# Kernel optimization log

Hardware: AMD Instinct MI355X
Metric: run time of the kernel (lower is better)

## Reference

```python
import jax, jax.numpy as jnp
import numpy as np

N_NODES = 100000
N_EDGES = 1600000
F_IN, F_HID, F_OUT = 48, 16, 16
K = 2  # kernel_size, dim=1, degree=1 open B-spline -> basis (1-u, u)


def glorot(key, shape):
    fan_in, fan_out = shape[-2], shape[-1]
    s = jnp.sqrt(6.0 / (fan_in + fan_out))
    return jax.random.uniform(key, shape, jnp.float32, -s, s)


def setup_inputs() -> dict:
    key = jax.random.key(0)
    ks = jax.random.split(key, 10)
    x = jax.random.normal(ks[0], (N_NODES, F_IN), jnp.float32)
    edge_attr = jax.random.uniform(ks[1], (N_EDGES, 1), jnp.float32)
    edge_index = jax.random.randint(ks[2], (2, N_EDGES), 0, N_NODES, jnp.int64)
    W1 = glorot(ks[3], (K, F_IN, F_HID))
    root1 = glorot(ks[4], (F_IN, F_HID))
    b1 = jnp.zeros((F_HID,), jnp.float32)
    W2 = glorot(ks[5], (K, F_HID, F_OUT))
    root2 = glorot(ks[6], (F_HID, F_OUT))
    b2 = jnp.zeros((F_OUT,), jnp.float32)
    return {"x": x, "edge_attr": edge_attr, "edge_index": edge_index,
            "W1": W1, "root1": root1, "b1": b1, "W2": W2, "root2": root2, "b2": b2}


def spline_conv(x, edge_index, u, W, root, bias, num_nodes):
    # x: [N,Fin], u: [E] pseudo coords in [0,1], W: [2,Fin,Fout]
    src, dst = edge_index[0], edge_index[1]
    xj = x[src]                                        # [E,Fin] gather
    m = jnp.einsum('ef,kfo->eko', xj, W)               # [E,2,Fout]
    basis = jnp.stack([1.0 - u, u], axis=1)            # linear open B-spline, K=2
    msg = jnp.einsum('ek,eko->eo', basis, m)           # [E,Fout]
    agg = jax.ops.segment_sum(msg, dst, num_segments=num_nodes)
    cnt = jax.ops.segment_sum(jnp.ones_like(msg[:, 0]), dst, num_segments=num_nodes)
    agg = agg / jnp.maximum(cnt, 1.0)[:, None]         # aggr='mean'
    return agg + x @ root + bias                       # root_weight + bias


def reference(x, edge_attr, edge_index, W1, root1, b1, W2, root2, b2):
    u = edge_attr[:, 0]
    h = jax.nn.elu(spline_conv(x, edge_index, u, W1, root1, b1, N_NODES))
    out = spline_conv(h, edge_index, u, W2, root2, b2, N_NODES)
    return jax.nn.log_softmax(out, axis=1)
```

## Files before the change

kernel.cpp:

```cpp
#include <hip/hip_runtime.h>
#include <math.h>

#define N_NODES 100000
#define N_EDGES 1600000
#define NBUK 782
#define BNODES 128
#define CAP 2560
#define CAPB (CAP * 8)
#define NCHUNK 512
#define CPE 3125
#define NTBLK 1563
#define WS 52
#define RPW (BNODES + 1)

#define SM_LCUR  0
#define SM_GBASE 3128
#define SM_SC    6256
#define SM_UPDL  10352
#define SM_SPDL  35352
#define SM_TOTAL 60352

#define NTL(p) __builtin_nontemporal_load(p)

__device__ __forceinline__ unsigned bf16_rne(float x) {
    unsigned u = __float_as_uint(x);
    return (u + 0x7FFFu + ((u >> 16) & 1u)) >> 16;
}

__device__ __forceinline__ void accq(float acc[4], uint4 w, float uu) {
    acc[0] += fmaf(uu, __uint_as_float(w.x & 0xFFFF0000u), __uint_as_float(w.x << 16));
    acc[1] += fmaf(uu, __uint_as_float(w.y & 0xFFFF0000u), __uint_as_float(w.y << 16));
    acc[2] += fmaf(uu, __uint_as_float(w.z & 0xFFFF0000u), __uint_as_float(w.z << 16));
    acc[3] += fmaf(uu, __uint_as_float(w.w & 0xFFFF0000u), __uint_as_float(w.w << 16));
}

__global__ __launch_bounds__(1024)
void fused_transform_scatter(const float* __restrict__ X,
                             const float* __restrict__ W,
                             const float* __restrict__ root,
                             const float* __restrict__ bias,
                             unsigned* __restrict__ YPH, float* __restrict__ R,
                             const int* __restrict__ src,
                             const int* __restrict__ dst,
                             const float* __restrict__ u,
                             int* __restrict__ cursor,
                             unsigned long long* __restrict__ pkd) {
    extern __shared__ char smem[];
    int t = threadIdx.x;
    if (blockIdx.x < NCHUNK) {
        int c = blockIdx.x;
        int* lcur = (int*)(smem + SM_LCUR);
        int* gbase = (int*)(smem + SM_GBASE);
        int* sc = (int*)(smem + SM_SC);
        unsigned long long* updl = (unsigned long long*)(smem + SM_UPDL);
        unsigned long long* spdl = (unsigned long long*)(smem + SM_SPDL);

        for (int i = t; i < NBUK; i += 1024) lcur[i] = 0;
        __syncthreads();
        for (int j = t; j < CPE; j += 1024) {
            int e = c * CPE + j;
            int d = NTL(dst + e);
            float uu = NTL(u + e);
            uu = uu < 0.0f ? 0.0f : (uu > 1.0f ? 1.0f : uu);
            int u15 = (int)fmaf(uu, 32767.0f, 0.5f);
            unsigned pk32 = (unsigned)NTL(src + e) | ((unsigned)u15 << 17);
            updl[j] = (unsigned long long)pk32 |
                      ((unsigned long long)(unsigned)d << 32);
            atomicAdd(&lcur[d >> 7], 1);
        }
        __syncthreads();

        int v = (t < NBUK) ? lcur[t] : 0;
        sc[t] = v;
        __syncthreads();
        for (int off = 1; off < 1024; off <<= 1) {
            int x = (t >= off) ? sc[t - off] : 0;
            __syncthreads();
            sc[t] += x;
            __syncthreads();
        }
        if (t < NBUK) {
            int ex = sc[t] - v;
            lcur[t] = ex;
            int base = t * CAP + atomicAdd(&cursor[t], v);
            gbase[t] = base - ex;
        }
        __syncthreads();

        for (int j = t; j < CPE; j += 1024) {
            unsigned long long w = updl[j];
            int b = (int)(w >> 39) & 0x3FF;
            int p = atomicAdd(&lcur[b], 1);
            spdl[p] = w;
        }
        __syncthreads();

        for (int j = t; j < CPE; j += 1024) {
            unsigned long long w = spdl[j];
            int b = (int)(w >> 39) & 0x3FF;
            int g = gbase[b] + j;
            if (g < (b + 1) * CAP)
                pkd[g] = w;
        }
    } else {
        float* sW0 = (float*)smem;
        float* sWd = (float*)(smem + 3328);
        float* sR  = (float*)(smem + 6656);
        float* sB  = (float*)(smem + 9984);
        int bid = blockIdx.x - NCHUNK;
        for (int i = t; i < 48 * 16; i += 1024) {
            int f = i >> 4, o = i & 15;
            float w0 = W[i];
            float w1 = W[48 * 16 + i];
            sW0[o * WS + f] = w0;
            sWd[o * WS + f] = w1 - w0;
            sR[o * WS + f]  = root[i];
        }
        if (t < 16) sB[t] = bias[t];
        __syncthreads();

        int idx = bid * 1024 + t;
        int n = idx >> 4;
        int o = idx & 15;
        if (n >= N_NODES) return;

        const float4* xr  = (const float4*)(X + (long)n * 48);
        const float4* w0p = (const float4*)(sW0 + o * WS);
        const float4* wdp = (const float4*)(sWd + o * WS);
        const float4* wrp = (const float4*)(sR  + o * WS);
        float a0 = 0.0f, a1 = 0.0f, ar = 0.0f;
#pragma unroll
        for (int fc = 0; fc < 12; ++fc) {
            float4 xv = xr[fc];
            float4 w0 = w0p[fc];
            float4 wd = wdp[fc];
            float4 wr = wrp[fc];
            a0 = fmaf(xv.x, w0.x, a0); a0 = fmaf(xv.y, w0.y, a0);
            a0 = fmaf(xv.z, w0.z, a0); a0 = fmaf(xv.w, w0.w, a0);
            a1 = fmaf(xv.x, wd.x, a1); a1 = fmaf(xv.y, wd.y, a1);
            a1 = fmaf(xv.z, wd.z, a1); a1 = fmaf(xv.w, wd.w, a1);
            ar = fmaf(xv.x, wr.x, ar); ar = fmaf(xv.y, wr.y, ar);
            ar = fmaf(xv.z, wr.z, ar); ar = fmaf(xv.w, wr.w, ar);
        }
        YPH[idx] = bf16_rne(a0) | (bf16_rne(a1) << 16);
        R[idx]   = ar + sB[o];
    }
}

__global__ __launch_bounds__(512)
void aggregate1(const int* __restrict__ cursor,
                unsigned long long* __restrict__ pkd,
                int* __restrict__ rptab,
                const uint4* __restrict__ YPH1,
                const float* __restrict__ R1,
                const float* __restrict__ W2,
                const float* __restrict__ root2,
                const float* __restrict__ b2,
                unsigned* __restrict__ YPH2,
                float* __restrict__ R2) {
    __shared__ unsigned long long updl[CAP];
    __shared__ unsigned spk[CAP];
    __shared__ int rp[RPW];
    __shared__ int cur[BNODES];
    __shared__ float sW0[256], sWd[256], sR[256], sB[16];
    int t = threadIdx.x, b = blockIdx.x;

    if (t < 256) {
        float w0 = W2[t], w1 = W2[256 + t];
        sW0[t] = w0;
        sWd[t] = w1 - w0;
        sR[t]  = root2[t];
    }
    if (t < 16) sB[t] = b2[t];
    if (t < BNODES) cur[t] = 0;
    __syncthreads();

    int cnt = cursor[b];
    if (cnt > CAP) cnt = CAP;
    unsigned long long* gp =
        (unsigned long long*)((char*)pkd + (size_t)b * CAPB);

    for (int j = t; j < cnt; j += 512) {
        unsigned long long w = NTL(gp + j);
        updl[j] = w;
        atomicAdd(&cur[(int)(w >> 32) & 127], 1);
    }
    __syncthreads();

    int v = 0;
    if (t < BNODES) { v = cur[t]; rp[t] = v; }
    __syncthreads();
    for (int off = 1; off < BNODES; off <<= 1) {
        int x = 0;
        if (t < BNODES && t >= off) x = rp[t - off];
        __syncthreads();
        if (t < BNODES) rp[t] += x;
        __syncthreads();
    }
    if (t < BNODES) { int ex = rp[t] - v; rp[t] = ex; cur[t] = ex; }
    if (t == 0) rp[BNODES] = cnt;
    __syncthreads();

    for (int j = t; j < cnt; j += 512) {
        unsigned long long w = updl[j];
        int pos = atomicAdd(&cur[(int)(w >> 32) & 127], 1);
        spk[pos] = (unsigned)w;
    }
    __syncthreads();

    unsigned* gs = (unsigned*)((char*)pkd + (size_t)b * CAPB);
    for (int j = t; j < cnt; j += 512) gs[j] = spk[j];
    if (t < RPW) rptab[b * RPW + t] = rp[t];

    int node = t >> 2, q = t & 3;
    int n = (b << 7) + node;
    int beg = rp[node], end = rp[node + 1];
    int deg = end - beg;
    const float C = 1.0f / 32767.0f;

    float acc[4] = {0.0f, 0.0f, 0.0f, 0.0f};
    int j = beg;
    for (; j + 3 < end; j += 4) {
        unsigned p0 = spk[j], p1 = spk[j + 1], p2 = spk[j + 2], p3 = spk[j + 3];
        uint4 w0 = YPH1[(size_t)(p0 & 0x1FFFFu) * 4 + q];
        uint4 w1 = YPH1[(size_t)(p1 & 0x1FFFFu) * 4 + q];
        uint4 w2 = YPH1[(size_t)(p2 & 0x1FFFFu) * 4 + q];
        uint4 w3 = YPH1[(size_t)(p3 & 0x1FFFFu) * 4 + q];
        accq(acc, w0, (float)(p0 >> 17) * C);
        accq(acc, w1, (float)(p1 >> 17) * C);
        accq(acc, w2, (float)(p2 >> 17) * C);
        accq(acc, w3, (float)(p3 >> 17) * C);
    }
    for (; j < end; ++j) {
        unsigned p = spk[j];
        uint4 w = YPH1[(size_t)(p & 0x1FFFFu) * 4 + q];
        accq(acc, w, (float)(p >> 17) * C);
    }

    if (n < N_NODES) {
        float inv = 1.0f / (deg > 0 ? (float)deg : 1.0f);
        float4 rr = ((const float4*)(R1 + (size_t)n * 16))[q];
        float hq[4], w;
        w = fmaf(acc[0], inv, rr.x); hq[0] = w > 0.0f ? w : expm1f(w);
        w = fmaf(acc[1], inv, rr.y); hq[1] = w > 0.0f ? w : expm1f(w);
        w = fmaf(acc[2], inv, rr.z); hq[2] = w > 0.0f ? w : expm1f(w);
        w = fmaf(acc[3], inv, rr.w); hq[3] = w > 0.0f ? w : expm1f(w);

        int qbase = (t & 63) & ~3;
        float h16[16];
#pragma unroll
        for (int p = 0; p < 4; ++p) {
            h16[4 * p + 0] = __shfl(hq[0], qbase + p);
            h16[4 * p + 1] = __shfl(hq[1], qbase + p);
            h16[4 * p + 2] = __shfl(hq[2], qbase + p);
            h16[4 * p + 3] = __shfl(hq[3], qbase + p);
        }

        float a0[4] = {0, 0, 0, 0}, a1[4] = {0, 0, 0, 0}, ar[4] = {0, 0, 0, 0};
        int o0 = q * 4;
#pragma unroll
        for (int f = 0; f < 16; ++f) {
            float hv = h16[f];
#pragma unroll
            for (int o = 0; o < 4; ++o) {
                a0[o] = fmaf(hv, sW0[f * 16 + o0 + o], a0[o]);
                a1[o] = fmaf(hv, sWd[f * 16 + o0 + o], a1[o]);
                ar[o] = fmaf(hv, sR [f * 16 + o0 + o], ar[o]);
            }
        }
        uint4 yw;
        yw.x = bf16_rne(a0[0]) | (bf16_rne(a1[0]) << 16);
        yw.y = bf16_rne(a0[1]) | (bf16_rne(a1[1]) << 16);
        yw.z = bf16_rne(a0[2]) | (bf16_rne(a1[2]) << 16);
        yw.w = bf16_rne(a0[3]) | (bf16_rne(a1[3]) << 16);
        ((uint4*)YPH2)[(size_t)n * 4 + q] = yw;
        float4 rv;
        rv.x = ar[0] + sB[o0 + 0];
        rv.y = ar[1] + sB[o0 + 1];
        rv.z = ar[2] + sB[o0 + 2];
        rv.w = ar[3] + sB[o0 + 3];
        ((float4*)R2)[(size_t)n * 4 + q] = rv;
    }
}

__global__ __launch_bounds__(512)
void aggregate2(const int* __restrict__ rptab,
                const unsigned long long* __restrict__ pkd,
                const uint4* __restrict__ YPH2,
                const float* __restrict__ R2,
                float* __restrict__ out) {
    __shared__ int rp[RPW];
    int t = threadIdx.x, b = blockIdx.x;

    if (t < RPW) rp[t] = rptab[b * RPW + t];
    __syncthreads();

    const unsigned* pk = (const unsigned*)((const char*)pkd + (size_t)b * CAPB);
    int node = t >> 2, q = t & 3;
    int n = (b << 7) + node;
    int beg = rp[node], end = rp[node + 1];
    int deg = end - beg;
    const float C = 1.0f / 32767.0f;

    float acc[4] = {0.0f, 0.0f, 0.0f, 0.0f};
    int j = beg;
    for (; j + 3 < end; j += 4) {
        unsigned p0 = NTL(pk + j), p1 = NTL(pk + j + 1);
        unsigned p2 = NTL(pk + j + 2), p3 = NTL(pk + j + 3);
        uint4 w0 = YPH2[(size_t)(p0 & 0x1FFFFu) * 4 + q];
        uint4 w1 = YPH2[(size_t)(p1 & 0x1FFFFu) * 4 + q];
        uint4 w2 = YPH2[(size_t)(p2 & 0x1FFFFu) * 4 + q];
        uint4 w3 = YPH2[(size_t)(p3 & 0x1FFFFu) * 4 + q];
        accq(acc, w0, (float)(p0 >> 17) * C);
        accq(acc, w1, (float)(p1 >> 17) * C);
        accq(acc, w2, (float)(p2 >> 17) * C);
        accq(acc, w3, (float)(p3 >> 17) * C);
    }
    for (; j < end; ++j) {
        unsigned p = NTL(pk + j);
        uint4 w = YPH2[(size_t)(p & 0x1FFFFu) * 4 + q];
        accq(acc, w, (float)(p >> 17) * C);
    }

    if (n < N_NODES) {
        float inv = 1.0f / (deg > 0 ? (float)deg : 1.0f);
        float4 rr = ((const float4*)R2)[(size_t)n * 4 + q];
        float v0 = fmaf(acc[0], inv, rr.x);
        float v1 = fmaf(acc[1], inv, rr.y);
        float v2 = fmaf(acc[2], inv, rr.z);
        float v3 = fmaf(acc[3], inv, rr.w);
        float m = fmaxf(fmaxf(v0, v1), fmaxf(v2, v3));
        m = fmaxf(m, __shfl_xor(m, 1));
        m = fmaxf(m, __shfl_xor(m, 2));
        float s = expf(v0 - m) + expf(v1 - m) + expf(v2 - m) + expf(v3 - m);
        s += __shfl_xor(s, 1);
        s += __shfl_xor(s, 2);
        float lse = m + logf(s);
        float4 ov = make_float4(v0 - lse, v1 - lse, v2 - lse, v3 - lse);
        ((float4*)out)[(size_t)n * 4 + q] = ov;
    }
}

extern "C" void kernel_launch(void* const* d_in, const int* in_sizes, int n_in,
                              void* d_out, int out_size, void* d_ws, size_t ws_size,
                              hipStream_t stream) {
    const float* x         = (const float*)d_in[0];
    const float* edge_attr = (const float*)d_in[1];
    const int*   edge_idx  = (const int*)d_in[2];
    const float* W1        = (const float*)d_in[3];
    const float* root1     = (const float*)d_in[4];
    const float* b1        = (const float*)d_in[5];
    const float* W2        = (const float*)d_in[6];
    const float* root2     = (const float*)d_in[7];
    const float* b2        = (const float*)d_in[8];
    float* out = (float*)d_out;

    const int* src = edge_idx;
    const int* dst = edge_idx + N_EDGES;

    char* ws = (char*)d_ws;
    unsigned long long* pkd = (unsigned long long*)(ws);
    unsigned* YPH1 = (unsigned*)(ws + 16015360);
    float*    R1   = (float*)(ws + 22415360);
    unsigned* YPH2 = (unsigned*)(ws + 28815360);
    float*    R2   = (float*)(ws + 35215360);
    int*      cursor = (int*)(ws + 41615360);
    int*      rptab  = (int*)(ws + 41618496);

    hipMemsetAsync(cursor, 0, NBUK * sizeof(int), stream);

    fused_transform_scatter<<<dim3(NCHUNK + NTBLK), 1024, SM_TOTAL, stream>>>(
        x, W1, root1, b1, YPH1, R1, src, dst, edge_attr, cursor, pkd);

    aggregate1<<<dim3(NBUK), 512, 0, stream>>>(
        cursor, pkd, rptab, (const uint4*)YPH1, R1, W2, root2, b2, YPH2, R2);

    aggregate2<<<dim3(NBUK), 512, 0, stream>>>(
        rptab, pkd, (const uint4*)YPH2, R2, out);
}
```

Measured before the change: 180.1 us.

## Split each aggregation bucket across two blocks and two lanes per feature quad

```diff
diff --git a/kernel.cpp b/kernel.cpp
--- a/kernel.cpp
+++ b/kernel.cpp
@@ -6,12 +6,12 @@
 #define NBUK 782
 #define BNODES 128
 #define CAP 2560
-#define CAPB (CAP * 8)
+#define NAGG (NBUK * 2)
 #define NCHUNK 512
 #define CPE 3125
 #define NTBLK 1563
 #define WS 52
-#define RPW (BNODES + 1)
+#define RPW 65
 
 #define SM_LCUR  0
 #define SM_GBASE 3128
@@ -149,7 +149,8 @@
 
 __global__ __launch_bounds__(512)
 void aggregate1(const int* __restrict__ cursor,
-                unsigned long long* __restrict__ pkd,
+                const unsigned long long* __restrict__ pkd,
+                unsigned* __restrict__ pks,
                 int* __restrict__ rptab,
                 const uint4* __restrict__ YPH1,
                 const float* __restrict__ R1,
@@ -161,9 +162,9 @@
     __shared__ unsigned long long updl[CAP];
     __shared__ unsigned spk[CAP];
     __shared__ int rp[RPW];
-    __shared__ int cur[BNODES];
+    __shared__ int cur[64];
     __shared__ float sW0[256], sWd[256], sR[256], sB[16];
-    int t = threadIdx.x, b = blockIdx.x;
+    int t = threadIdx.x, bb = blockIdx.x, b = bb >> 1, hh = bb & 1;
 
     if (t < 256) {
         float w0 = W2[t], w1 = W2[256 + t];
@@ -172,56 +173,66 @@
         sR[t]  = root2[t];
     }
     if (t < 16) sB[t] = b2[t];
-    if (t < BNODES) cur[t] = 0;
+    if (t < 64) cur[t] = 0;
     __syncthreads();
 
     int cnt = cursor[b];
     if (cnt > CAP) cnt = CAP;
-    unsigned long long* gp =
-        (unsigned long long*)((char*)pkd + (size_t)b * CAPB);
+    const unsigned long long* gp = pkd + (size_t)b * CAP;
 
     for (int j = t; j < cnt; j += 512) {
         unsigned long long w = NTL(gp + j);
         updl[j] = w;
-        atomicAdd(&cur[(int)(w >> 32) & 127], 1);
+        int node = (int)(w >> 32) & 127;
+        if ((node >> 6) == hh) atomicAdd(&cur[node & 63], 1);
     }
     __syncthreads();
 
     int v = 0;
-    if (t < BNODES) { v = cur[t]; rp[t] = v; }
-    __syncthreads();
-    for (int off = 1; off < BNODES; off <<= 1) {
+    if (t < 64) { v = cur[t]; rp[t] = v; }
+    __syncthreads();
+    for (int off = 1; off < 64; off <<= 1) {
         int x = 0;
-        if (t < BNODES && t >= off) x = rp[t - off];
-        __syncthreads();
-        if (t < BNODES) rp[t] += x;
-        __syncthreads();
-    }
-    if (t < BNODES) { int ex = rp[t] - v; rp[t] = ex; cur[t] = ex; }
-    if (t == 0) rp[BNODES] = cnt;
+        if (t < 64 && t >= off) x = rp[t - off];
+        __syncthreads();
+        if (t < 64) rp[t] += x;
+        __syncthreads();
+    }
+    if (t < 64) {
+        int ex = rp[t] - v;
+        rp[t] = ex;
+        cur[t] = ex;
+        if (t == 63) rp[64] = ex + v;
+    }
     __syncthreads();
 
     for (int j = t; j < cnt; j += 512) {
         unsigned long long w = updl[j];
-        int pos = atomicAdd(&cur[(int)(w >> 32) & 127], 1);
-        spk[pos] = (unsigned)w;
-    }
-    __syncthreads();
-
-    unsigned* gs = (unsigned*)((char*)pkd + (size_t)b * CAPB);
-    for (int j = t; j < cnt; j += 512) gs[j] = spk[j];
-    if (t < RPW) rptab[b * RPW + t] = rp[t];
-
-    int node = t >> 2, q = t & 3;
-    int n = (b << 7) + node;
-    int beg = rp[node], end = rp[node + 1];
+        int node = (int)(w >> 32) & 127;
+        if ((node >> 6) == hh) {
+            int pos = atomicAdd(&cur[node & 63], 1);
+            spk[pos] = (unsigned)w;
+        }
+    }
+    __syncthreads();
+
+    int cown = rp[64];
+    int base = hh ? (cnt - cown) : 0;
+
+    unsigned* gw = pks + (size_t)b * CAP + base;
+    for (int j = t; j < cown; j += 512) gw[j] = spk[j];
+    if (t < RPW) rptab[bb * RPW + t] = base + rp[t];
+
+    int node64 = t >> 3, lane3 = t & 7, q = lane3 & 3, h = lane3 >> 2;
+    int n = (b << 7) + (hh << 6) + node64;
+    int beg = rp[node64], end = rp[node64 + 1];
     int deg = end - beg;
     const float C = 1.0f / 32767.0f;
 
     float acc[4] = {0.0f, 0.0f, 0.0f, 0.0f};
-    int j = beg;
-    for (; j + 3 < end; j += 4) {
-        unsigned p0 = spk[j], p1 = spk[j + 1], p2 = spk[j + 2], p3 = spk[j + 3];
+    int j = beg + h;
+    for (; j + 6 < end; j += 8) {
+        unsigned p0 = spk[j], p1 = spk[j + 2], p2 = spk[j + 4], p3 = spk[j + 6];
         uint4 w0 = YPH1[(size_t)(p0 & 0x1FFFFu) * 4 + q];
         uint4 w1 = YPH1[(size_t)(p1 & 0x1FFFFu) * 4 + q];
         uint4 w2 = YPH1[(size_t)(p2 & 0x1FFFFu) * 4 + q];
@@ -231,11 +242,13 @@
         accq(acc, w2, (float)(p2 >> 17) * C);
         accq(acc, w3, (float)(p3 >> 17) * C);
     }
-    for (; j < end; ++j) {
+    for (; j < end; j += 2) {
         unsigned p = spk[j];
         uint4 w = YPH1[(size_t)(p & 0x1FFFFu) * 4 + q];
         accq(acc, w, (float)(p >> 17) * C);
     }
+#pragma unroll
+    for (int i = 0; i < 4; ++i) acc[i] += __shfl_xor(acc[i], 4);
 
     if (n < N_NODES) {
         float inv = 1.0f / (deg > 0 ? (float)deg : 1.0f);
@@ -246,14 +259,14 @@
         w = fmaf(acc[2], inv, rr.z); hq[2] = w > 0.0f ? w : expm1f(w);
         w = fmaf(acc[3], inv, rr.w); hq[3] = w > 0.0f ? w : expm1f(w);
 
-        int qbase = (t & 63) & ~3;
+        int b8 = (t & 63) & ~7;
         float h16[16];
 #pragma unroll
         for (int p = 0; p < 4; ++p) {
-            h16[4 * p + 0] = __shfl(hq[0], qbase + p);
-            h16[4 * p + 1] = __shfl(hq[1], qbase + p);
-            h16[4 * p + 2] = __shfl(hq[2], qbase + p);
-            h16[4 * p + 3] = __shfl(hq[3], qbase + p);
+            h16[4 * p + 0] = __shfl(hq[0], b8 + p);
+            h16[4 * p + 1] = __shfl(hq[1], b8 + p);
+            h16[4 * p + 2] = __shfl(hq[2], b8 + p);
+            h16[4 * p + 3] = __shfl(hq[3], b8 + p);
         }
 
         float a0[4] = {0, 0, 0, 0}, a1[4] = {0, 0, 0, 0}, ar[4] = {0, 0, 0, 0};
@@ -268,45 +281,47 @@
                 ar[o] = fmaf(hv, sR [f * 16 + o0 + o], ar[o]);
             }
         }
-        uint4 yw;
-        yw.x = bf16_rne(a0[0]) | (bf16_rne(a1[0]) << 16);
-        yw.y = bf16_rne(a0[1]) | (bf16_rne(a1[1]) << 16);
-        yw.z = bf16_rne(a0[2]) | (bf16_rne(a1[2]) << 16);
-        yw.w = bf16_rne(a0[3]) | (bf16_rne(a1[3]) << 16);
-        ((uint4*)YPH2)[(size_t)n * 4 + q] = yw;
-        float4 rv;
-        rv.x = ar[0] + sB[o0 + 0];
-        rv.y = ar[1] + sB[o0 + 1];
-        rv.z = ar[2] + sB[o0 + 2];
-        rv.w = ar[3] + sB[o0 + 3];
-        ((float4*)R2)[(size_t)n * 4 + q] = rv;
+        if (h == 0) {
+            uint4 yw;
+            yw.x = bf16_rne(a0[0]) | (bf16_rne(a1[0]) << 16);
+            yw.y = bf16_rne(a0[1]) | (bf16_rne(a1[1]) << 16);
+            yw.z = bf16_rne(a0[2]) | (bf16_rne(a1[2]) << 16);
+            yw.w = bf16_rne(a0[3]) | (bf16_rne(a1[3]) << 16);
+            ((uint4*)YPH2)[(size_t)n * 4 + q] = yw;
+            float4 rv;
+            rv.x = ar[0] + sB[o0 + 0];
+            rv.y = ar[1] + sB[o0 + 1];
+            rv.z = ar[2] + sB[o0 + 2];
+            rv.w = ar[3] + sB[o0 + 3];
+            ((float4*)R2)[(size_t)n * 4 + q] = rv;
+        }
     }
 }
 
 __global__ __launch_bounds__(512)
 void aggregate2(const int* __restrict__ rptab,
-                const unsigned long long* __restrict__ pkd,
+                const unsigned* __restrict__ pks,
                 const uint4* __restrict__ YPH2,
                 const float* __restrict__ R2,
                 float* __restrict__ out) {
     __shared__ int rp[RPW];
-    int t = threadIdx.x, b = blockIdx.x;
-
-    if (t < RPW) rp[t] = rptab[b * RPW + t];
-    __syncthreads();
-
-    const unsigned* pk = (const unsigned*)((const char*)pkd + (size_t)b * CAPB);
-    int node = t >> 2, q = t & 3;
-    int n = (b << 7) + node;
-    int beg = rp[node], end = rp[node + 1];
+    int t = threadIdx.x, bb = blockIdx.x, b = bb >> 1, hh = bb & 1;
+
+    if (t < RPW) rp[t] = rptab[bb * RPW + t];
+    __syncthreads();
+
+    const unsigned* pk = pks + (size_t)b * CAP;
+    int node64 = t >> 3, lane3 = t & 7, q = lane3 & 3, h = lane3 >> 2;
+    int n = (b << 7) + (hh << 6) + node64;
+    int beg = rp[node64], end = rp[node64 + 1];
     int deg = end - beg;
     const float C = 1.0f / 32767.0f;
 
     float acc[4] = {0.0f, 0.0f, 0.0f, 0.0f};
-    int j = beg;
-    for (; j + 3 < end; j += 4) {
-        unsigned p0 = NTL(pk + j), p1 = NTL(pk + j + 1);
-        unsigned p2 = NTL(pk + j + 2), p3 = NTL(pk + j + 3);
+    int j = beg + h;
+    for (; j + 6 < end; j += 8) {
+        unsigned p0 = NTL(pk + j), p1 = NTL(pk + j + 2);
+        unsigned p2 = NTL(pk + j + 4), p3 = NTL(pk + j + 6);
         uint4 w0 = YPH2[(size_t)(p0 & 0x1FFFFu) * 4 + q];
         uint4 w1 = YPH2[(size_t)(p1 & 0x1FFFFu) * 4 + q];
         uint4 w2 = YPH2[(size_t)(p2 & 0x1FFFFu) * 4 + q];
@@ -316,11 +331,13 @@
         accq(acc, w2, (float)(p2 >> 17) * C);
         accq(acc, w3, (float)(p3 >> 17) * C);
     }
-    for (; j < end; ++j) {
+    for (; j < end; j += 2) {
         unsigned p = NTL(pk + j);
         uint4 w = YPH2[(size_t)(p & 0x1FFFFu) * 4 + q];
         accq(acc, w, (float)(p >> 17) * C);
     }
+#pragma unroll
+    for (int i = 0; i < 4; ++i) acc[i] += __shfl_xor(acc[i], 4);
 
     if (n < N_NODES) {
         float inv = 1.0f / (deg > 0 ? (float)deg : 1.0f);
@@ -336,8 +353,10 @@
         s += __shfl_xor(s, 1);
         s += __shfl_xor(s, 2);
         float lse = m + logf(s);
-        float4 ov = make_float4(v0 - lse, v1 - lse, v2 - lse, v3 - lse);
-        ((float4*)out)[(size_t)n * 4 + q] = ov;
+        if (h == 0) {
+            float4 ov = make_float4(v0 - lse, v1 - lse, v2 - lse, v3 - lse);
+            ((float4*)out)[(size_t)n * 4 + q] = ov;
+        }
     }
 }
 
@@ -360,21 +379,22 @@
 
     char* ws = (char*)d_ws;
     unsigned long long* pkd = (unsigned long long*)(ws);
-    unsigned* YPH1 = (unsigned*)(ws + 16015360);
-    float*    R1   = (float*)(ws + 22415360);
-    unsigned* YPH2 = (unsigned*)(ws + 28815360);
-    float*    R2   = (float*)(ws + 35215360);
-    int*      cursor = (int*)(ws + 41615360);
-    int*      rptab  = (int*)(ws + 41618496);
+    unsigned* pks  = (unsigned*)(ws + 16015360);
+    unsigned* YPH1 = (unsigned*)(ws + 24023040);
+    float*    R1   = (float*)(ws + 30423040);
+    unsigned* YPH2 = (unsigned*)(ws + 36823040);
+    float*    R2   = (float*)(ws + 43223040);
+    int*      cursor = (int*)(ws + 49623040);
+    int*      rptab  = (int*)(ws + 49626176);
 
     hipMemsetAsync(cursor, 0, NBUK * sizeof(int), stream);
 
     fused_transform_scatter<<<dim3(NCHUNK + NTBLK), 1024, SM_TOTAL, stream>>>(
         x, W1, root1, b1, YPH1, R1, src, dst, edge_attr, cursor, pkd);
 
-    aggregate1<<<dim3(NBUK), 512, 0, stream>>>(
-        cursor, pkd, rptab, (const uint4*)YPH1, R1, W2, root2, b2, YPH2, R2);
-
-    aggregate2<<<dim3(NBUK), 512, 0, stream>>>(
-        rptab, pkd, (const uint4*)YPH2, R2, out);
-}
+    aggregate1<<<dim3(NAGG), 512, 0, stream>>>(
+        cursor, pkd, pks, rptab, (const uint4*)YPH1, R1, W2, root2, b2, YPH2, R2);
+
+    aggregate2<<<dim3(NAGG), 512, 0, stream>>>(
+        rptab, pks, (const uint4*)YPH2, R2, out);
+}
```

Result: slower. 185.4 us (+2.9%).
